# Kernel tuning notes

Hardware: AMD Instinct MI355X
Metric: run time of the kernel (lower is better)

## Reference

```python
import jax, jax.numpy as jnp
import numpy as np

SQRT2 = 1.4142135623730951
TARGET_DENSITY = 0.9
XL, YL, XH, YH = 0.0, 0.0, 1024.0, 1024.0
BSX, BSY = 2.0, 2.0
NM, NT, NF = 1_000_000, 10_000, 200_000
N_TOTAL = NM + NT + NF
NBX = int(round((XH - XL) / BSX))  # 512
NBY = int(round((YH - YL) / BSY))  # 512
K_MOV = 5   # ceil((max movable size 3 + 2*sqrt2*bs) / bs) with bs=2
K_FIX = 10  # ceil((max fixed size 16 + bs) / bs) with margin; extra bins overlap 0
PADDING = 1


def _splat(x, y, sx, sy, w, K):
    """Scatter-add exact rectangle/bin overlaps of each cell into a flat [NBX*NBY] map.
    x,y: lower-left corners [N]; sx,sy: sizes [N]; w: per-cell weight (ratio) [N]."""
    bx0 = jnp.floor((x - XL) / BSX).astype(jnp.int32)  # first impacted bin in x
    by0 = jnp.floor((y - YL) / BSY).astype(jnp.int32)
    ks = jnp.arange(K, dtype=jnp.int32)
    bx = bx0[:, None] + ks  # [N,K]
    by = by0[:, None] + ks
    ox = jnp.minimum(x[:, None] + sx[:, None], XL + (bx + 1) * BSX) - \
         jnp.maximum(x[:, None], XL + bx * BSX)
    oy = jnp.minimum(y[:, None] + sy[:, None], YL + (by + 1) * BSY) - \
         jnp.maximum(y[:, None], YL + by * BSY)
    ox = jnp.where((bx >= 0) & (bx < NBX), jnp.clip(ox, 0.0), 0.0)
    oy = jnp.where((by >= 0) & (by < NBY), jnp.clip(oy, 0.0), 0.0)
    bxc = jnp.clip(bx, 0, NBX - 1)
    byc = jnp.clip(by, 0, NBY - 1)
    v = w[:, None, None] * ox[:, :, None] * oy[:, None, :]        # [N,K,K]
    idx = (bxc[:, :, None] * NBY + byc[:, None, :]).reshape(-1)   # [N*K*K]
    return jnp.zeros(NBX * NBY, dtype=x.dtype).at[idx].add(v.reshape(-1))


def setup_inputs() -> dict:
    key = jax.random.key(0)
    k1, k2, k3, k4, k5, k6, k7, k8 = jax.random.split(key, 8)
    # node sizes: movable standard cells, fixed terminals (larger), fillers
    sx = jnp.concatenate([
        jax.random.uniform(k1, (NM,), minval=1.0, maxval=3.0),
        jax.random.uniform(k2, (NT,), minval=4.0, maxval=16.0),
        jax.random.uniform(k3, (NF,), minval=1.5, maxval=2.5)])
    sy = jnp.concatenate([
        jax.random.uniform(k4, (NM,), minval=1.0, maxval=3.0),
        jax.random.uniform(k5, (NT,), minval=4.0, maxval=16.0),
        jax.random.uniform(k6, (NF,), minval=1.5, maxval=2.5)])
    pos_x = jax.random.uniform(k7, (N_TOTAL,), minval=XL, maxval=XH - 16.0)
    pos_y = jax.random.uniform(k8, (N_TOTAL,), minval=YL, maxval=YH - 16.0)
    pos = jnp.concatenate([pos_x, pos_y])  # x coords then y coords
    return {"pos": pos, "node_size_x": sx, "node_size_y": sy}


def reference(pos, node_size_x, node_size_y):
    x = pos[:N_TOTAL]
    y = pos[N_TOTAL:]
    # --- initial density map from fixed terminals (exact overlap, no stretching) ---
    tsl = slice(NM, NM + NT)
    init_map = _splat(x[tsl], y[tsl], node_size_x[tsl], node_size_y[tsl],
                      jnp.ones((NT,), pos.dtype), K_FIX) * TARGET_DENSITY
    # --- movable + filler: stretch to >= bin_size*sqrt2, splat rescaled area ---
    sxc = jnp.maximum(node_size_x, BSX * SQRT2)
    syc = jnp.maximum(node_size_y, BSY * SQRT2)
    off_x = (node_size_x - sxc) * 0.5
    off_y = (node_size_y - syc) * 0.5
    ratio = (node_size_x * node_size_y) / (sxc * syc)
    mf = np.concatenate([np.arange(NM), np.arange(N_TOTAL - NF, N_TOTAL)])  # movable + filler
    dmap = init_map + _splat((x + off_x)[mf], (y + off_y)[mf], sxc[mf], syc[mf],
                             ratio[mf], K_MOV)
    dmap = dmap.reshape(NBX, NBY)
    # padding mask: border bins forced to target capacity
    bin_area = BSX * BSY
    ix = jnp.arange(NBX)
    iy = jnp.arange(NBY)
    pad = ((ix < PADDING) | (ix >= NBX - PADDING))[:, None] | \
          ((iy < PADDING) | (iy >= NBY - PADDING))[None, :]
    dmap = jnp.where(pad, TARGET_DENSITY * bin_area, dmap)
    density_cost = jnp.clip(dmap - TARGET_DENSITY * bin_area, 0.0).sum()[None]
    max_density = (dmap.max() / bin_area)[None]
    return density_cost, max_density
```

## Files before the change

kernel.cpp:

```cpp
#include <hip/hip_runtime.h>

#define NM_ 1000000
#define NT_ 10000
#define NF_ 200000
#define N_TOTAL_ 1210000
#define NBX_ 512
#define NBY_ 512
#define NBINS_ (NBX_ * NBY_)
#define TD_ 0.9f
#define PAD_VAL_ 3.6f
#define SQRT2x2_ 2.8284271247461903f

#define TSZ_ 16
#define TSH_ 4
#define TGX_ 32
#define NTILES_ 1024
#define HALO_ 2
#define TW_ 18
#define TAREA_ (TW_ * TW_)
#define CAPM_ 1536
#define CAPT_ 128
#define NB_ 512
#define NTH_ 512
#define CHUNK_ 2364
#define NGRP_ 8
#define QS_ 1024.0f
#define IQS_ (1.0f / 1024.0f)

static __device__ __forceinline__ int imin_(int a, int b) { return a < b ? a : b; }
static __device__ __forceinline__ int imax_(int a, int b) { return a > b ? a : b; }

static __device__ __forceinline__ void fadd_(float* p, float v) {
    unsafeAtomicAdd(p, v);
}

__global__ __launch_bounds__(NTH_) void count_kernel(
        const float* __restrict__ px, const float* __restrict__ py,
        const float* __restrict__ sxp, const float* __restrict__ syp,
        int* __restrict__ cnt, int* __restrict__ cntT) {
    __shared__ int hist[NTILES_];
    for (int t = threadIdx.x; t < NTILES_; t += blockDim.x) hist[t] = 0;
    if (blockIdx.x == 0)
        for (int t = threadIdx.x; t < NTILES_; t += blockDim.x) cntT[t] = 0;
    __syncthreads();
    int b = blockIdx.x;
    int lo = b * CHUNK_, hi = imin_(lo + CHUNK_, N_TOTAL_);
    for (int i = lo + threadIdx.x; i < hi; i += blockDim.x) {
        if (i >= NM_ && i < NM_ + NT_) continue;
        float sx0 = sxp[i], sy0 = syp[i];
        float sxc = fmaxf(sx0, SQRT2x2_);
        float syc = fmaxf(sy0, SQRT2x2_);
        float x = px[i] + (sx0 - sxc) * 0.5f;
        float y = py[i] + (sy0 - syc) * 0.5f;
        int bx0 = (int)floorf(x * 0.5f);
        int by0 = (int)floorf(y * 0.5f);
        int t = (imax_(bx0, 0) >> TSH_) * TGX_ + (imax_(by0, 0) >> TSH_);
        atomicAdd(&hist[t], 1);
    }
    __syncthreads();
    for (int t = threadIdx.x; t < NTILES_; t += blockDim.x)
        cnt[b * NTILES_ + t] = hist[t];
}

__global__ void scan_kernel(int* __restrict__ cnt, int* __restrict__ totM,
                            float* __restrict__ out) {
    int tile = blockIdx.x * 4 + (threadIdx.x >> 6);
    int l = threadIdx.x & 63;
    int X = l & 7;
    int mrow = l >> 3;
    int c[NGRP_];
#pragma unroll
    for (int g = 0; g < NGRP_; g++) c[g] = cnt[(l + 64 * g) * NTILES_ + tile];
    int off[NGRP_];
    int W = 0;
#pragma unroll
    for (int g = 0; g < NGRP_; g++) {
        int v = c[g];
#pragma unroll
        for (int s = 1; s < 8; s <<= 1) {
            int n = __shfl_up(v, 8 * s);
            if (mrow >= s) v += n;
        }
        off[g] = W + v - c[g];
        W += __shfl(v, X + 56);
    }
    int B = 0, tot = 0;
#pragma unroll
    for (int Xp = 0; Xp < 8; Xp++) {
        int t = __shfl(W, Xp);
        if (Xp < X) B += t;
        tot += t;
    }
#pragma unroll
    for (int g = 0; g < NGRP_; g++) cnt[(l + 64 * g) * NTILES_ + tile] = B + off[g];
    if (l == 0) totM[tile] = tot;
    if (blockIdx.x == 0 && threadIdx.x == 0) { out[0] = 0.0f; out[1] = 0.0f; }
}

__global__ __launch_bounds__(NTH_) void scatter_kernel(
        const float* __restrict__ px, const float* __restrict__ py,
        const float* __restrict__ sxp, const float* __restrict__ syp,
        const int* __restrict__ start, int* __restrict__ cntT,
        ushort4* __restrict__ recM, unsigned char* __restrict__ keyM,
        float4* __restrict__ recT) {
    __shared__ int cur[NTILES_];
    int b = blockIdx.x;
    for (int t = threadIdx.x; t < NTILES_; t += blockDim.x)
        cur[t] = start[b * NTILES_ + t];
    __syncthreads();
    int lo = b * CHUNK_, hi = imin_(lo + CHUNK_, N_TOTAL_);
    for (int i = lo + threadIdx.x; i < hi; i += blockDim.x) {
        float sx0 = sxp[i], sy0 = syp[i];
        bool fix = (i >= NM_) && (i < NM_ + NT_);
        if (!fix) {
            float sxc = fmaxf(sx0, SQRT2x2_);
            float syc = fmaxf(sy0, SQRT2x2_);
            float x = px[i] + (sx0 - sxc) * 0.5f;
            float y = py[i] + (sy0 - syc) * 0.5f;
            int bx0 = (int)floorf(x * 0.5f);
            int by0 = (int)floorf(y * 0.5f);
            int txo = (imax_(bx0, 0) >> TSH_) << TSH_;
            int tyo = (imax_(by0, 0) >> TSH_) << TSH_;
            int t = (txo >> TSH_) * TGX_ + (tyo >> TSH_);
            int slot = atomicAdd(&cur[t], 1);
            if (slot < CAPM_) {
                float bxo = txo * 2.0f - 16.0f;
                float byo = tyo * 2.0f - 16.0f;
                ushort4 q;
                q.x = (unsigned short)__float2int_rn((x - bxo) * QS_);
                q.y = (unsigned short)__float2int_rn((y - byo) * QS_);
                q.z = (unsigned short)__float2int_rn(sx0 * QS_);
                q.w = (unsigned short)__float2int_rn(sy0 * QS_);
                recM[(size_t)t * CAPM_ + slot] = q;
                int kr = imin_(imax_(bx0 - txo, 0), 15);
                int kc = imin_(imax_(by0 - tyo, 0), 15);
                keyM[(size_t)t * CAPM_ + slot] = (unsigned char)(kr * 16 + kc);
            }
        } else {
            float x = px[i], y = py[i];
            int bx0 = (int)floorf(x * 0.5f);
            int by0 = (int)floorf(y * 0.5f);
            int bxm = imin_((int)floorf((x + sx0) * 0.5f), NBX_ - 1);
            int bym = imin_((int)floorf((y + sy0) * 0.5f), NBY_ - 1);
            int txA = bx0 >> TSH_, txB = bxm >> TSH_;
            int tyA = by0 >> TSH_, tyB = bym >> TSH_;
            for (int tx = txA; tx <= txB; tx++)
                for (int ty = tyA; ty <= tyB; ty++) {
                    int t = tx * TGX_ + ty;
                    int slot = atomicAdd(&cntT[t], 1);
                    if (slot < CAPT_) recT[(size_t)t * CAPT_ + slot] = make_float4(x, y, sx0, sy0);
                }
        }
    }
}

__global__ __launch_bounds__(512) void accumS_kernel(
        const ushort4* __restrict__ recM, const unsigned char* __restrict__ keyM,
        const float4* __restrict__ recT,
        const int* __restrict__ totM, const int* __restrict__ cntT,
        float* __restrict__ tiles) {
    __shared__ float4 srec[CAPM_];
    __shared__ float  sw[CAPM_];
    __shared__ float  m[TAREA_];
    __shared__ int    boff[257];
    __shared__ int    bcur[256];
    int tile = blockIdx.x;
    int tx16 = (tile >> 5) << TSH_;
    int ty16 = (tile & (TGX_ - 1)) << TSH_;
    for (int k = threadIdx.x; k < TAREA_; k += 512) m[k] = 0.0f;
    if (threadIdx.x < 256) bcur[threadIdx.x] = 0;
    __syncthreads();
    int nM = imin_(totM[tile], CAPM_);
    const ushort4* rq = recM + (size_t)tile * CAPM_;
    const unsigned char* kM = keyM + (size_t)tile * CAPM_;
    for (int i = threadIdx.x; i < nM; i += 512)
        atomicAdd(&bcur[kM[i]], 1);
    __syncthreads();
    if (threadIdx.x < 64) {
        int l = threadIdx.x;
        int c0 = bcur[4 * l], c1 = bcur[4 * l + 1], c2 = bcur[4 * l + 2], c3 = bcur[4 * l + 3];
        int s = c0 + c1 + c2 + c3;
        int incl = s;
#pragma unroll
        for (int off = 1; off < 64; off <<= 1) {
            int n = __shfl_up(incl, off);
            if (l >= off) incl += n;
        }
        int run = incl - s;
        boff[4 * l] = run;
        boff[4 * l + 1] = run + c0;
        boff[4 * l + 2] = run + c0 + c1;
        boff[4 * l + 3] = run + c0 + c1 + c2;
        if (l == 63) boff[256] = incl;
    }
    __syncthreads();
    if (threadIdx.x < 256) bcur[threadIdx.x] = boff[threadIdx.x];
    __syncthreads();
    float bxo = tx16 * 2.0f - 16.0f;
    float byo = ty16 * 2.0f - 16.0f;
    for (int i = threadIdx.x; i < nM; i += 512) {
        ushort4 q = rq[i];
        float x = bxo + q.x * IQS_;
        float y = byo + q.y * IQS_;
        float sx0 = q.z * IQS_, sy0 = q.w * IQS_;
        float sxc = fmaxf(sx0, SQRT2x2_);
        float syc = fmaxf(sy0, SQRT2x2_);
        float w = (sx0 * sy0) / (sxc * syc);
        int slot = atomicAdd(&bcur[kM[i]], 1);
        srec[slot] = make_float4(x, y, x + sxc, y + syc);
        sw[slot] = w;
    }
    int nT = imin_(cntT[tile], CAPT_);
    const float4* rT = recT + (size_t)tile * CAPT_;
    for (int i = threadIdx.x; i < nT; i += 512) {
        float4 r = rT[i];
        float xe = r.x + r.z, ye = r.y + r.w;
        int bx0 = (int)floorf(r.x * 0.5f);
        int by0 = (int)floorf(r.y * 0.5f);
        int bxA = imax_(bx0, tx16), byA = imax_(by0, ty16);
        int bxB = imin_(imin_((int)floorf(xe * 0.5f), tx16 + TSZ_ - 1), NBX_ - 1);
        int byB = imin_(imin_((int)floorf(ye * 0.5f), ty16 + TSZ_ - 1), NBY_ - 1);
        for (int bx = bxA; bx <= bxB; bx++) {
            float ox = fminf(xe, (bx + 1) * 2.0f) - fmaxf(r.x, bx * 2.0f);
            ox = fmaxf(ox, 0.0f) * TD_;
            for (int by = byA; by <= byB; by++) {
                float oy = fminf(ye, (by + 1) * 2.0f) - fmaxf(r.y, by * 2.0f);
                atomicAdd(&m[(bx - tx16) * TW_ + (by - ty16)], ox * fmaxf(oy, 0.0f));
            }
        }
    }
    __syncthreads();
    if (threadIdx.x < TAREA_) {
        int r = threadIdx.x / TW_;
        int c = threadIdx.x % TW_;
        float blx = (tx16 + r) * 2.0f, bhx = blx + 2.0f;
        float bly = (ty16 + c) * 2.0f, bhy = bly + 2.0f;
        int krA = imax_(r - 2, 0), krB = imin_(r, 15);
        int kcA = imax_(c - 2, 0), kcB = imin_(c, 15);
        float acc = 0.0f;
        for (int kr = krA; kr <= krB; kr++) {
            int j0 = boff[kr * 16 + kcA];
            int j1 = boff[kr * 16 + kcB + 1];
            for (int j = j0; j < j1; j++) {
                float4 t = srec[j];
                float ox = fminf(t.z, bhx) - fmaxf(t.x, blx);
                float oy = fminf(t.w, bhy) - fmaxf(t.y, bly);
                acc = fmaf(sw[j], fmaxf(ox, 0.0f) * fmaxf(oy, 0.0f), acc);
            }
        }
        m[threadIdx.x] += acc;
    }
    __syncthreads();
    for (int k = threadIdx.x; k < TAREA_; k += 512)
        tiles[(size_t)tile * TAREA_ + k] = m[k];
}

__global__ void reduce2_kernel(const float* __restrict__ tiles, float* __restrict__ out) {
    float sum = 0.0f, mx = 0.0f;
    for (int i = blockIdx.x * blockDim.x + threadIdx.x; i < NBINS_;
         i += gridDim.x * blockDim.x) {
        int gx = i >> 9, gy = i & (NBY_ - 1);
        float v;
        bool pad = (gx < 1) | (gx >= NBX_ - 1) | (gy < 1) | (gy >= NBY_ - 1);
        if (pad) {
            v = PAD_VAL_;
        } else {
            int tx = gx >> TSH_, lx = gx & (TSZ_ - 1);
            int ty = gy >> TSH_, ly = gy & (TSZ_ - 1);
            v = tiles[(size_t)(tx * TGX_ + ty) * TAREA_ + lx * TW_ + ly];
            if (lx < HALO_ && tx > 0)
                v += tiles[(size_t)((tx - 1) * TGX_ + ty) * TAREA_ + (lx + TSZ_) * TW_ + ly];
            if (ly < HALO_ && ty > 0)
                v += tiles[(size_t)(tx * TGX_ + (ty - 1)) * TAREA_ + lx * TW_ + (ly + TSZ_)];
            if (lx < HALO_ && ly < HALO_ && tx > 0 && ty > 0)
                v += tiles[(size_t)((tx - 1) * TGX_ + (ty - 1)) * TAREA_ + (lx + TSZ_) * TW_ + (ly + TSZ_)];
        }
        sum += fmaxf(v - PAD_VAL_, 0.0f);
        mx = fmaxf(mx, v);
    }
#pragma unroll
    for (int off = 32; off > 0; off >>= 1) {
        sum += __shfl_down(sum, off);
        mx = fmaxf(mx, __shfl_down(mx, off));
    }
    __shared__ float ssum[8], smx[8];
    int lane = threadIdx.x & 63, wid = threadIdx.x >> 6;
    if (lane == 0) { ssum[wid] = sum; smx[wid] = mx; }
    __syncthreads();
    if (threadIdx.x == 0) {
        int nw = blockDim.x >> 6;
        float s = 0.0f, m = 0.0f;
        for (int w = 0; w < nw; w++) { s += ssum[w]; m = fmaxf(m, smx[w]); }
        fadd_(&out[0], s);
        atomicMax((unsigned int*)&out[1], __float_as_uint(m * 0.25f));
    }
}

__global__ void zero_kernel(float* __restrict__ dmap, float* __restrict__ out) {
    int i = blockIdx.x * blockDim.x + threadIdx.x;
    if (i < NBINS_) dmap[i] = 0.0f;
    if (i == 0) { out[0] = 0.0f; out[1] = 0.0f; }
}

__global__ void splat_fix(const float* __restrict__ px, const float* __restrict__ py,
                          const float* __restrict__ sxp, const float* __restrict__ syp,
                          float* __restrict__ dmap) {
    int t = blockIdx.x * blockDim.x + threadIdx.x;
    if (t >= NT_) return;
    int i = NM_ + t;
    float x = px[i], y = py[i], sx = sxp[i], sy = syp[i];
    int bx0 = (int)floorf(x * 0.5f), by0 = (int)floorf(y * 0.5f);
    for (int kx = 0; kx < 10; kx++) {
        int bx = bx0 + kx;
        if (bx < 0 || bx >= NBX_) continue;
        float ox = fminf(x + sx, (bx + 1) * 2.0f) - fmaxf(x, bx * 2.0f);
        if (ox <= 0.0f) continue;
        for (int ky = 0; ky < 10; ky++) {
            int by = by0 + ky;
            if (by < 0 || by >= NBY_) continue;
            float oy = fminf(y + sy, (by + 1) * 2.0f) - fmaxf(y, by * 2.0f);
            if (oy <= 0.0f) continue;
            fadd_(&dmap[bx * NBY_ + by], TD_ * ox * oy);
        }
    }
}

__global__ void splat_mov(const float* __restrict__ px, const float* __restrict__ py,
                          const float* __restrict__ sxp, const float* __restrict__ syp,
                          float* __restrict__ dmap) {
    int i = blockIdx.x * blockDim.x + threadIdx.x;
    if (i >= N_TOTAL_) return;
    if (i >= NM_ && i < NM_ + NT_) return;
    float sx = sxp[i], sy = syp[i];
    float sxc = fmaxf(sx, SQRT2x2_), syc = fmaxf(sy, SQRT2x2_);
    float x = px[i] + (sx - sxc) * 0.5f, y = py[i] + (sy - syc) * 0.5f;
    float w = (sx * sy) / (sxc * syc);
    int bx0 = (int)floorf(x * 0.5f), by0 = (int)floorf(y * 0.5f);
    for (int kx = 0; kx < 5; kx++) {
        int bx = bx0 + kx;
        if (bx < 0 || bx >= NBX_) continue;
        float ox = fminf(x + sxc, (bx + 1) * 2.0f) - fmaxf(x, bx * 2.0f);
        if (ox <= 0.0f) continue;
        for (int ky = 0; ky < 5; ky++) {
            int by = by0 + ky;
            if (by < 0 || by >= NBY_) continue;
            float oy = fminf(y + syc, (by + 1) * 2.0f) - fmaxf(y, by * 2.0f);
            if (oy <= 0.0f) continue;
            fadd_(&dmap[bx * NBY_ + by], w * ox * oy);
        }
    }
}

__global__ void reduce_kernel(const float* __restrict__ dmap, float* __restrict__ out) {
    float sum = 0.0f, mx = 0.0f;
    for (int i = blockIdx.x * blockDim.x + threadIdx.x; i < NBINS_;
         i += gridDim.x * blockDim.x) {
        int ix = i >> 9, iy = i & (NBY_ - 1);
        float v = dmap[i];
        bool pad = (ix < 1) | (ix >= NBX_ - 1) | (iy < 1) | (iy >= NBY_ - 1);
        if (pad) v = PAD_VAL_;
        sum += fmaxf(v - PAD_VAL_, 0.0f);
        mx = fmaxf(mx, v);
    }
#pragma unroll
    for (int off = 32; off > 0; off >>= 1) {
        sum += __shfl_down(sum, off);
        mx = fmaxf(mx, __shfl_down(mx, off));
    }
    __shared__ float ssum[8], smx[8];
    int lane = threadIdx.x & 63, wid = threadIdx.x >> 6;
    if (lane == 0) { ssum[wid] = sum; smx[wid] = mx; }
    __syncthreads();
    if (threadIdx.x == 0) {
        int nw = blockDim.x >> 6;
        float s = 0.0f, m = 0.0f;
        for (int w = 0; w < nw; w++) { s += ssum[w]; m = fmaxf(m, smx[w]); }
        fadd_(&out[0], s);
        atomicMax((unsigned int*)&out[1], __float_as_uint(m * 0.25f));
    }
}

extern "C" void kernel_launch(void* const* d_in, const int* in_sizes, int n_in,
                              void* d_out, int out_size, void* d_ws, size_t ws_size,
                              hipStream_t stream) {
    const float* pos = (const float*)d_in[0];
    const float* nsx = (const float*)d_in[1];
    const float* nsy = (const float*)d_in[2];
    const float* px = pos;
    const float* py = pos + N_TOTAL_;
    float* out = (float*)d_out;

    size_t o_cnt   = 0;
    size_t o_totM  = o_cnt + (size_t)NB_ * NTILES_ * 4;
    size_t o_cntT  = o_totM + (size_t)NTILES_ * 4;
    size_t o_recM  = o_cntT + (size_t)NTILES_ * 4;
    size_t o_keyM  = o_recM + (size_t)NTILES_ * CAPM_ * 8;
    size_t o_recT  = o_keyM + (size_t)NTILES_ * CAPM_;
    size_t o_tiles = o_recT + (size_t)NTILES_ * CAPT_ * 16;
    size_t req     = o_tiles + (size_t)NTILES_ * TAREA_ * 4;

    if (ws_size >= req) {
        char* ws = (char*)d_ws;
        int*           cnt   = (int*)(ws + o_cnt);
        int*           totM  = (int*)(ws + o_totM);
        int*           cntT  = (int*)(ws + o_cntT);
        ushort4*       recM  = (ushort4*)(ws + o_recM);
        unsigned char* keyM  = (unsigned char*)(ws + o_keyM);
        float4*        recT  = (float4*)(ws + o_recT);
        float*         tiles = (float*)(ws + o_tiles);

        count_kernel<<<NB_, NTH_, 0, stream>>>(px, py, nsx, nsy, cnt, cntT);
        scan_kernel<<<NTILES_ / 4, 256, 0, stream>>>(cnt, totM, out);
        scatter_kernel<<<NB_, NTH_, 0, stream>>>(px, py, nsx, nsy, cnt, cntT, recM, keyM, recT);
        accumS_kernel<<<NTILES_, 512, 0, stream>>>(recM, keyM, recT, totM, cntT, tiles);
        reduce2_kernel<<<1024, 256, 0, stream>>>(tiles, out);
    } else {
        float* dmap = (float*)d_ws;
        zero_kernel<<<(NBINS_ + 255) / 256, 256, 0, stream>>>(dmap, out);
        splat_fix<<<(NT_ + 255) / 256, 256, 0, stream>>>(px, py, nsx, nsy, dmap);
        splat_mov<<<(N_TOTAL_ + 255) / 256, 256, 0, stream>>>(px, py, nsx, nsy, dmap);
        reduce_kernel<<<1024, 256, 0, stream>>>(dmap, out);
    }
}
```

Before: 91.40 us.

## Replace count+scan+scatter with single-pass per-block segmented tile buckets

```diff
diff --git a/kernel.cpp b/kernel.cpp
--- a/kernel.cpp
+++ b/kernel.cpp
@@ -23,7 +23,7 @@
 #define NB_ 512
 #define NTH_ 512
 #define CHUNK_ 2364
-#define NGRP_ 8
+#define SEGC_ 16
 #define QS_ 1024.0f
 #define IQS_ (1.0f / 1024.0f)
 
@@ -34,80 +34,21 @@
     unsafeAtomicAdd(p, v);
 }
 
-__global__ __launch_bounds__(NTH_) void count_kernel(
+__global__ void zero0_kernel(int* __restrict__ cntT, float* __restrict__ out) {
+    int i = blockIdx.x * blockDim.x + threadIdx.x;
+    if (i < NTILES_) cntT[i] = 0;
+    if (i == 0) { out[0] = 0.0f; out[1] = 0.0f; }
+}
+
+__global__ __launch_bounds__(NTH_) void scatter1_kernel(
         const float* __restrict__ px, const float* __restrict__ py,
         const float* __restrict__ sxp, const float* __restrict__ syp,
-        int* __restrict__ cnt, int* __restrict__ cntT) {
-    __shared__ int hist[NTILES_];
-    for (int t = threadIdx.x; t < NTILES_; t += blockDim.x) hist[t] = 0;
-    if (blockIdx.x == 0)
-        for (int t = threadIdx.x; t < NTILES_; t += blockDim.x) cntT[t] = 0;
+        int* __restrict__ cnt, int* __restrict__ cntT,
+        ushort4* __restrict__ recM, float4* __restrict__ recT) {
+    __shared__ int cur[NTILES_];
+    for (int t = threadIdx.x; t < NTILES_; t += blockDim.x) cur[t] = 0;
     __syncthreads();
     int b = blockIdx.x;
-    int lo = b * CHUNK_, hi = imin_(lo + CHUNK_, N_TOTAL_);
-    for (int i = lo + threadIdx.x; i < hi; i += blockDim.x) {
-        if (i >= NM_ && i < NM_ + NT_) continue;
-        float sx0 = sxp[i], sy0 = syp[i];
-        float sxc = fmaxf(sx0, SQRT2x2_);
-        float syc = fmaxf(sy0, SQRT2x2_);
-        float x = px[i] + (sx0 - sxc) * 0.5f;
-        float y = py[i] + (sy0 - syc) * 0.5f;
-        int bx0 = (int)floorf(x * 0.5f);
-        int by0 = (int)floorf(y * 0.5f);
-        int t = (imax_(bx0, 0) >> TSH_) * TGX_ + (imax_(by0, 0) >> TSH_);
-        atomicAdd(&hist[t], 1);
-    }
-    __syncthreads();
-    for (int t = threadIdx.x; t < NTILES_; t += blockDim.x)
-        cnt[b * NTILES_ + t] = hist[t];
-}
-
-__global__ void scan_kernel(int* __restrict__ cnt, int* __restrict__ totM,
-                            float* __restrict__ out) {
-    int tile = blockIdx.x * 4 + (threadIdx.x >> 6);
-    int l = threadIdx.x & 63;
-    int X = l & 7;
-    int mrow = l >> 3;
-    int c[NGRP_];
-#pragma unroll
-    for (int g = 0; g < NGRP_; g++) c[g] = cnt[(l + 64 * g) * NTILES_ + tile];
-    int off[NGRP_];
-    int W = 0;
-#pragma unroll
-    for (int g = 0; g < NGRP_; g++) {
-        int v = c[g];
-#pragma unroll
-        for (int s = 1; s < 8; s <<= 1) {
-            int n = __shfl_up(v, 8 * s);
-            if (mrow >= s) v += n;
-        }
-        off[g] = W + v - c[g];
-        W += __shfl(v, X + 56);
-    }
-    int B = 0, tot = 0;
-#pragma unroll
-    for (int Xp = 0; Xp < 8; Xp++) {
-        int t = __shfl(W, Xp);
-        if (Xp < X) B += t;
-        tot += t;
-    }
-#pragma unroll
-    for (int g = 0; g < NGRP_; g++) cnt[(l + 64 * g) * NTILES_ + tile] = B + off[g];
-    if (l == 0) totM[tile] = tot;
-    if (blockIdx.x == 0 && threadIdx.x == 0) { out[0] = 0.0f; out[1] = 0.0f; }
-}
-
-__global__ __launch_bounds__(NTH_) void scatter_kernel(
-        const float* __restrict__ px, const float* __restrict__ py,
-        const float* __restrict__ sxp, const float* __restrict__ syp,
-        const int* __restrict__ start, int* __restrict__ cntT,
-        ushort4* __restrict__ recM, unsigned char* __restrict__ keyM,
-        float4* __restrict__ recT) {
-    __shared__ int cur[NTILES_];
-    int b = blockIdx.x;
-    for (int t = threadIdx.x; t < NTILES_; t += blockDim.x)
-        cur[t] = start[b * NTILES_ + t];
-    __syncthreads();
     int lo = b * CHUNK_, hi = imin_(lo + CHUNK_, N_TOTAL_);
     for (int i = lo + threadIdx.x; i < hi; i += blockDim.x) {
         float sx0 = sxp[i], sy0 = syp[i];
@@ -123,7 +64,7 @@
             int tyo = (imax_(by0, 0) >> TSH_) << TSH_;
             int t = (txo >> TSH_) * TGX_ + (tyo >> TSH_);
             int slot = atomicAdd(&cur[t], 1);
-            if (slot < CAPM_) {
+            if (slot < SEGC_) {
                 float bxo = txo * 2.0f - 16.0f;
                 float byo = tyo * 2.0f - 16.0f;
                 ushort4 q;
@@ -131,10 +72,7 @@
                 q.y = (unsigned short)__float2int_rn((y - byo) * QS_);
                 q.z = (unsigned short)__float2int_rn(sx0 * QS_);
                 q.w = (unsigned short)__float2int_rn(sy0 * QS_);
-                recM[(size_t)t * CAPM_ + slot] = q;
-                int kr = imin_(imax_(bx0 - txo, 0), 15);
-                int kc = imin_(imax_(by0 - tyo, 0), 15);
-                keyM[(size_t)t * CAPM_ + slot] = (unsigned char)(kr * 16 + kc);
+                recM[((size_t)t * NB_ + b) * SEGC_ + slot] = q;
             }
         } else {
             float x = px[i], y = py[i];
@@ -152,29 +90,40 @@
                 }
         }
     }
-}
-
-__global__ __launch_bounds__(512) void accumS_kernel(
-        const ushort4* __restrict__ recM, const unsigned char* __restrict__ keyM,
-        const float4* __restrict__ recT,
-        const int* __restrict__ totM, const int* __restrict__ cntT,
+    __syncthreads();
+    for (int t = threadIdx.x; t < NTILES_; t += blockDim.x)
+        cnt[b * NTILES_ + t] = imin_(cur[t], SEGC_);
+}
+
+__global__ __launch_bounds__(512) void accumSeg_kernel(
+        const ushort4* __restrict__ recM, const float4* __restrict__ recT,
+        const int* __restrict__ cnt, const int* __restrict__ cntT,
         float* __restrict__ tiles) {
     __shared__ float4 srec[CAPM_];
     __shared__ float  sw[CAPM_];
     __shared__ float  m[TAREA_];
     __shared__ int    boff[257];
     __shared__ int    bcur[256];
+    __shared__ unsigned char scnt[NB_];
     int tile = blockIdx.x;
     int tx16 = (tile >> 5) << TSH_;
     int ty16 = (tile & (TGX_ - 1)) << TSH_;
     for (int k = threadIdx.x; k < TAREA_; k += 512) m[k] = 0.0f;
     if (threadIdx.x < 256) bcur[threadIdx.x] = 0;
-    __syncthreads();
-    int nM = imin_(totM[tile], CAPM_);
-    const ushort4* rq = recM + (size_t)tile * CAPM_;
-    const unsigned char* kM = keyM + (size_t)tile * CAPM_;
-    for (int i = threadIdx.x; i < nM; i += 512)
-        atomicAdd(&bcur[kM[i]], 1);
+    if (threadIdx.x < NB_) scnt[threadIdx.x] = (unsigned char)cnt[threadIdx.x * NTILES_ + tile];
+    __syncthreads();
+    const ushort4* seg0 = recM + (size_t)tile * NB_ * SEGC_;
+    {
+        int b = threadIdx.x;
+        int c = scnt[b];
+        const ushort4* p = seg0 + b * SEGC_;
+        for (int j = 0; j < c; j++) {
+            ushort4 q = p[j];
+            int kr = imin_(imax_((q.x >> 11) - 8, 0), 15);
+            int kc = imin_(imax_((q.y >> 11) - 8, 0), 15);
+            atomicAdd(&bcur[kr * 16 + kc], 1);
+        }
+    }
     __syncthreads();
     if (threadIdx.x < 64) {
         int l = threadIdx.x;
@@ -198,17 +147,26 @@
     __syncthreads();
     float bxo = tx16 * 2.0f - 16.0f;
     float byo = ty16 * 2.0f - 16.0f;
-    for (int i = threadIdx.x; i < nM; i += 512) {
-        ushort4 q = rq[i];
-        float x = bxo + q.x * IQS_;
-        float y = byo + q.y * IQS_;
-        float sx0 = q.z * IQS_, sy0 = q.w * IQS_;
-        float sxc = fmaxf(sx0, SQRT2x2_);
-        float syc = fmaxf(sy0, SQRT2x2_);
-        float w = (sx0 * sy0) / (sxc * syc);
-        int slot = atomicAdd(&bcur[kM[i]], 1);
-        srec[slot] = make_float4(x, y, x + sxc, y + syc);
-        sw[slot] = w;
+    {
+        int b = threadIdx.x;
+        int c = scnt[b];
+        const ushort4* p = seg0 + b * SEGC_;
+        for (int j = 0; j < c; j++) {
+            ushort4 q = p[j];
+            int kr = imin_(imax_((q.x >> 11) - 8, 0), 15);
+            int kc = imin_(imax_((q.y >> 11) - 8, 0), 15);
+            float x = bxo + q.x * IQS_;
+            float y = byo + q.y * IQS_;
+            float sx0 = q.z * IQS_, sy0 = q.w * IQS_;
+            float sxc = fmaxf(sx0, SQRT2x2_);
+            float syc = fmaxf(sy0, SQRT2x2_);
+            float w = (sx0 * sy0) / (sxc * syc);
+            int slot = atomicAdd(&bcur[kr * 16 + kc], 1);
+            if (slot < CAPM_) {
+                srec[slot] = make_float4(x, y, x + sxc, y + syc);
+                sw[slot] = w;
+            }
+        }
     }
     int nT = imin_(cntT[tile], CAPT_);
     const float4* rT = recT + (size_t)tile * CAPT_;
@@ -239,8 +197,8 @@
         int kcA = imax_(c - 2, 0), kcB = imin_(c, 15);
         float acc = 0.0f;
         for (int kr = krA; kr <= krB; kr++) {
-            int j0 = boff[kr * 16 + kcA];
-            int j1 = boff[kr * 16 + kcB + 1];
+            int j0 = imin_(boff[kr * 16 + kcA], CAPM_);
+            int j1 = imin_(boff[kr * 16 + kcB + 1], CAPM_);
             for (int j = j0; j < j1; j++) {
                 float4 t = srec[j];
                 float ox = fminf(t.z, bhx) - fmaxf(t.x, blx);
@@ -391,28 +349,23 @@
     float* out = (float*)d_out;
 
     size_t o_cnt   = 0;
-    size_t o_totM  = o_cnt + (size_t)NB_ * NTILES_ * 4;
-    size_t o_cntT  = o_totM + (size_t)NTILES_ * 4;
+    size_t o_cntT  = o_cnt + (size_t)NB_ * NTILES_ * 4;
     size_t o_recM  = o_cntT + (size_t)NTILES_ * 4;
-    size_t o_keyM  = o_recM + (size_t)NTILES_ * CAPM_ * 8;
-    size_t o_recT  = o_keyM + (size_t)NTILES_ * CAPM_;
+    size_t o_recT  = o_recM + (size_t)NTILES_ * NB_ * SEGC_ * 8;
     size_t o_tiles = o_recT + (size_t)NTILES_ * CAPT_ * 16;
     size_t req     = o_tiles + (size_t)NTILES_ * TAREA_ * 4;
 
     if (ws_size >= req) {
         char* ws = (char*)d_ws;
-        int*           cnt   = (int*)(ws + o_cnt);
-        int*           totM  = (int*)(ws + o_totM);
-        int*           cntT  = (int*)(ws + o_cntT);
-        ushort4*       recM  = (ushort4*)(ws + o_recM);
-        unsigned char* keyM  = (unsigned char*)(ws + o_keyM);
-        float4*        recT  = (float4*)(ws + o_recT);
-        float*         tiles = (float*)(ws + o_tiles);
-
-        count_kernel<<<NB_, NTH_, 0, stream>>>(px, py, nsx, nsy, cnt, cntT);
-        scan_kernel<<<NTILES_ / 4, 256, 0, stream>>>(cnt, totM, out);
-        scatter_kernel<<<NB_, NTH_, 0, stream>>>(px, py, nsx, nsy, cnt, cntT, recM, keyM, recT);
-        accumS_kernel<<<NTILES_, 512, 0, stream>>>(recM, keyM, recT, totM, cntT, tiles);
+        int*     cnt   = (int*)(ws + o_cnt);
+        int*     cntT  = (int*)(ws + o_cntT);
+        ushort4* recM  = (ushort4*)(ws + o_recM);
+        float4*  recT  = (float4*)(ws + o_recT);
+        float*   tiles = (float*)(ws + o_tiles);
+
+        zero0_kernel<<<4, 256, 0, stream>>>(cntT, out);
+        scatter1_kernel<<<NB_, NTH_, 0, stream>>>(px, py, nsx, nsy, cnt, cntT, recM, recT);
+        accumSeg_kernel<<<NTILES_, 512, 0, stream>>>(recM, recT, cnt, cntT, tiles);
         reduce2_kernel<<<1024, 256, 0, stream>>>(tiles, out);
     } else {
         float* dmap = (float*)d_ws;
```

Result: slower. 102.6 us (+12.3%).

## Split scatter into movable and fixed kernels, derive bin keys from quantized records

Applied to the files above, without the earlier changes.

```diff
diff --git a/kernel.cpp b/kernel.cpp
--- a/kernel.cpp
+++ b/kernel.cpp
@@ -34,14 +34,18 @@
     unsafeAtomicAdd(p, v);
 }
 
+__global__ void zero0_kernel(int* __restrict__ cntT, float* __restrict__ out) {
+    int i = blockIdx.x * blockDim.x + threadIdx.x;
+    if (i < NTILES_) cntT[i] = 0;
+    if (i == 0) { out[0] = 0.0f; out[1] = 0.0f; }
+}
+
 __global__ __launch_bounds__(NTH_) void count_kernel(
         const float* __restrict__ px, const float* __restrict__ py,
         const float* __restrict__ sxp, const float* __restrict__ syp,
-        int* __restrict__ cnt, int* __restrict__ cntT) {
+        int* __restrict__ cnt) {
     __shared__ int hist[NTILES_];
     for (int t = threadIdx.x; t < NTILES_; t += blockDim.x) hist[t] = 0;
-    if (blockIdx.x == 0)
-        for (int t = threadIdx.x; t < NTILES_; t += blockDim.x) cntT[t] = 0;
     __syncthreads();
     int b = blockIdx.x;
     int lo = b * CHUNK_, hi = imin_(lo + CHUNK_, N_TOTAL_);
@@ -62,8 +66,7 @@
         cnt[b * NTILES_ + t] = hist[t];
 }
 
-__global__ void scan_kernel(int* __restrict__ cnt, int* __restrict__ totM,
-                            float* __restrict__ out) {
+__global__ void scan_kernel(int* __restrict__ cnt, int* __restrict__ totM) {
     int tile = blockIdx.x * 4 + (threadIdx.x >> 6);
     int l = threadIdx.x & 63;
     int X = l & 7;
@@ -94,71 +97,73 @@
 #pragma unroll
     for (int g = 0; g < NGRP_; g++) cnt[(l + 64 * g) * NTILES_ + tile] = B + off[g];
     if (l == 0) totM[tile] = tot;
-    if (blockIdx.x == 0 && threadIdx.x == 0) { out[0] = 0.0f; out[1] = 0.0f; }
-}
-
-__global__ __launch_bounds__(NTH_) void scatter_kernel(
+}
+
+__global__ __launch_bounds__(NTH_) void scatterM_kernel(
         const float* __restrict__ px, const float* __restrict__ py,
         const float* __restrict__ sxp, const float* __restrict__ syp,
-        const int* __restrict__ start, int* __restrict__ cntT,
-        ushort4* __restrict__ recM, unsigned char* __restrict__ keyM,
-        float4* __restrict__ recT) {
+        const int* __restrict__ start, ushort4* __restrict__ recM) {
     __shared__ int cur[NTILES_];
     int b = blockIdx.x;
     for (int t = threadIdx.x; t < NTILES_; t += blockDim.x)
         cur[t] = start[b * NTILES_ + t];
     __syncthreads();
     int lo = b * CHUNK_, hi = imin_(lo + CHUNK_, N_TOTAL_);
-    for (int i = lo + threadIdx.x; i < hi; i += blockDim.x) {
+#pragma unroll 2
+    for (int i = lo + threadIdx.x; i < hi; i += NTH_) {
+        if (i >= NM_ && i < NM_ + NT_) continue;
         float sx0 = sxp[i], sy0 = syp[i];
-        bool fix = (i >= NM_) && (i < NM_ + NT_);
-        if (!fix) {
-            float sxc = fmaxf(sx0, SQRT2x2_);
-            float syc = fmaxf(sy0, SQRT2x2_);
-            float x = px[i] + (sx0 - sxc) * 0.5f;
-            float y = py[i] + (sy0 - syc) * 0.5f;
-            int bx0 = (int)floorf(x * 0.5f);
-            int by0 = (int)floorf(y * 0.5f);
-            int txo = (imax_(bx0, 0) >> TSH_) << TSH_;
-            int tyo = (imax_(by0, 0) >> TSH_) << TSH_;
-            int t = (txo >> TSH_) * TGX_ + (tyo >> TSH_);
-            int slot = atomicAdd(&cur[t], 1);
-            if (slot < CAPM_) {
-                float bxo = txo * 2.0f - 16.0f;
-                float byo = tyo * 2.0f - 16.0f;
-                ushort4 q;
-                q.x = (unsigned short)__float2int_rn((x - bxo) * QS_);
-                q.y = (unsigned short)__float2int_rn((y - byo) * QS_);
-                q.z = (unsigned short)__float2int_rn(sx0 * QS_);
-                q.w = (unsigned short)__float2int_rn(sy0 * QS_);
-                recM[(size_t)t * CAPM_ + slot] = q;
-                int kr = imin_(imax_(bx0 - txo, 0), 15);
-                int kc = imin_(imax_(by0 - tyo, 0), 15);
-                keyM[(size_t)t * CAPM_ + slot] = (unsigned char)(kr * 16 + kc);
-            }
-        } else {
-            float x = px[i], y = py[i];
-            int bx0 = (int)floorf(x * 0.5f);
-            int by0 = (int)floorf(y * 0.5f);
-            int bxm = imin_((int)floorf((x + sx0) * 0.5f), NBX_ - 1);
-            int bym = imin_((int)floorf((y + sy0) * 0.5f), NBY_ - 1);
-            int txA = bx0 >> TSH_, txB = bxm >> TSH_;
-            int tyA = by0 >> TSH_, tyB = bym >> TSH_;
-            for (int tx = txA; tx <= txB; tx++)
-                for (int ty = tyA; ty <= tyB; ty++) {
-                    int t = tx * TGX_ + ty;
-                    int slot = atomicAdd(&cntT[t], 1);
-                    if (slot < CAPT_) recT[(size_t)t * CAPT_ + slot] = make_float4(x, y, sx0, sy0);
-                }
-        }
-    }
+        float sxc = fmaxf(sx0, SQRT2x2_);
+        float syc = fmaxf(sy0, SQRT2x2_);
+        float x = px[i] + (sx0 - sxc) * 0.5f;
+        float y = py[i] + (sy0 - syc) * 0.5f;
+        int bx0 = (int)floorf(x * 0.5f);
+        int by0 = (int)floorf(y * 0.5f);
+        int txo = (imax_(bx0, 0) >> TSH_) << TSH_;
+        int tyo = (imax_(by0, 0) >> TSH_) << TSH_;
+        int t = (txo >> TSH_) * TGX_ + (tyo >> TSH_);
+        int slot = atomicAdd(&cur[t], 1);
+        if (slot < CAPM_) {
+            float bxo = txo * 2.0f - 16.0f;
+            float byo = tyo * 2.0f - 16.0f;
+            ushort4 q;
+            q.x = (unsigned short)__float2int_rn((x - bxo) * QS_);
+            q.y = (unsigned short)__float2int_rn((y - byo) * QS_);
+            q.z = (unsigned short)__float2int_rn(sx0 * QS_);
+            q.w = (unsigned short)__float2int_rn(sy0 * QS_);
+            recM[(size_t)t * CAPM_ + slot] = q;
+        }
+    }
+}
+
+__global__ void scatterT_kernel(
+        const float* __restrict__ px, const float* __restrict__ py,
+        const float* __restrict__ sxp, const float* __restrict__ syp,
+        int* __restrict__ cntT, float4* __restrict__ recT) {
+    int k = blockIdx.x * blockDim.x + threadIdx.x;
+    if (k >= NT_) return;
+    int i = NM_ + k;
+    float x = px[i], y = py[i];
+    float sx0 = sxp[i], sy0 = syp[i];
+    int bx0 = (int)floorf(x * 0.5f);
+    int by0 = (int)floorf(y * 0.5f);
+    int bxm = imin_((int)floorf((x + sx0) * 0.5f), NBX_ - 1);
+    int bym = imin_((int)floorf((y + sy0) * 0.5f), NBY_ - 1);
+    int txA = bx0 >> TSH_, txB = bxm >> TSH_;
+    int tyA = by0 >> TSH_, tyB = bym >> TSH_;
+    for (int tx = txA; tx <= txB; tx++)
+        for (int ty = tyA; ty <= tyB; ty++) {
+            int t = tx * TGX_ + ty;
+            int slot = atomicAdd(&cntT[t], 1);
+            if (slot < CAPT_) recT[(size_t)t * CAPT_ + slot] = make_float4(x, y, sx0, sy0);
+        }
 }
 
 __global__ __launch_bounds__(512) void accumS_kernel(
-        const ushort4* __restrict__ recM, const unsigned char* __restrict__ keyM,
-        const float4* __restrict__ recT,
+        const ushort4* __restrict__ recM, const float4* __restrict__ recT,
         const int* __restrict__ totM, const int* __restrict__ cntT,
         float* __restrict__ tiles) {
+    __shared__ ushort4 raw[CAPM_];
     __shared__ float4 srec[CAPM_];
     __shared__ float  sw[CAPM_];
     __shared__ float  m[TAREA_];
@@ -172,9 +177,13 @@
     __syncthreads();
     int nM = imin_(totM[tile], CAPM_);
     const ushort4* rq = recM + (size_t)tile * CAPM_;
-    const unsigned char* kM = keyM + (size_t)tile * CAPM_;
-    for (int i = threadIdx.x; i < nM; i += 512)
-        atomicAdd(&bcur[kM[i]], 1);
+    for (int i = threadIdx.x; i < nM; i += 512) {
+        ushort4 q = rq[i];
+        raw[i] = q;
+        int kr = imin_(imax_((q.x >> 11) - 8, 0), 15);
+        int kc = imin_(imax_((q.y >> 11) - 8, 0), 15);
+        atomicAdd(&bcur[kr * 16 + kc], 1);
+    }
     __syncthreads();
     if (threadIdx.x < 64) {
         int l = threadIdx.x;
@@ -199,14 +208,16 @@
     float bxo = tx16 * 2.0f - 16.0f;
     float byo = ty16 * 2.0f - 16.0f;
     for (int i = threadIdx.x; i < nM; i += 512) {
-        ushort4 q = rq[i];
+        ushort4 q = raw[i];
+        int kr = imin_(imax_((q.x >> 11) - 8, 0), 15);
+        int kc = imin_(imax_((q.y >> 11) - 8, 0), 15);
         float x = bxo + q.x * IQS_;
         float y = byo + q.y * IQS_;
         float sx0 = q.z * IQS_, sy0 = q.w * IQS_;
         float sxc = fmaxf(sx0, SQRT2x2_);
         float syc = fmaxf(sy0, SQRT2x2_);
         float w = (sx0 * sy0) / (sxc * syc);
-        int slot = atomicAdd(&bcur[kM[i]], 1);
+        int slot = atomicAdd(&bcur[kr * 16 + kc], 1);
         srec[slot] = make_float4(x, y, x + sxc, y + syc);
         sw[slot] = w;
     }
@@ -394,25 +405,25 @@
     size_t o_totM  = o_cnt + (size_t)NB_ * NTILES_ * 4;
     size_t o_cntT  = o_totM + (size_t)NTILES_ * 4;
     size_t o_recM  = o_cntT + (size_t)NTILES_ * 4;
-    size_t o_keyM  = o_recM + (size_t)NTILES_ * CAPM_ * 8;
-    size_t o_recT  = o_keyM + (size_t)NTILES_ * CAPM_;
+    size_t o_recT  = o_recM + (size_t)NTILES_ * CAPM_ * 8;
     size_t o_tiles = o_recT + (size_t)NTILES_ * CAPT_ * 16;
     size_t req     = o_tiles + (size_t)NTILES_ * TAREA_ * 4;
 
     if (ws_size >= req) {
         char* ws = (char*)d_ws;
-        int*           cnt   = (int*)(ws + o_cnt);
-        int*           totM  = (int*)(ws + o_totM);
-        int*           cntT  = (int*)(ws + o_cntT);
-        ushort4*       recM  = (ushort4*)(ws + o_recM);
-        unsigned char* keyM  = (unsigned char*)(ws + o_keyM);
-        float4*        recT  = (float4*)(ws + o_recT);
-        float*         tiles = (float*)(ws + o_tiles);
-
-        count_kernel<<<NB_, NTH_, 0, stream>>>(px, py, nsx, nsy, cnt, cntT);
-        scan_kernel<<<NTILES_ / 4, 256, 0, stream>>>(cnt, totM, out);
-        scatter_kernel<<<NB_, NTH_, 0, stream>>>(px, py, nsx, nsy, cnt, cntT, recM, keyM, recT);
-        accumS_kernel<<<NTILES_, 512, 0, stream>>>(recM, keyM, recT, totM, cntT, tiles);
+        int*     cnt   = (int*)(ws + o_cnt);
+        int*     totM  = (int*)(ws + o_totM);
+        int*     cntT  = (int*)(ws + o_cntT);
+        ushort4* recM  = (ushort4*)(ws + o_recM);
+        float4*  recT  = (float4*)(ws + o_recT);
+        float*   tiles = (float*)(ws + o_tiles);
+
+        zero0_kernel<<<4, 256, 0, stream>>>(cntT, out);
+        count_kernel<<<NB_, NTH_, 0, stream>>>(px, py, nsx, nsy, cnt);
+        scan_kernel<<<NTILES_ / 4, 256, 0, stream>>>(cnt, totM);
+        scatterM_kernel<<<NB_, NTH_, 0, stream>>>(px, py, nsx, nsy, cnt, recM);
+        scatterT_kernel<<<(NT_ + 255) / 256, 256, 0, stream>>>(px, py, nsx, nsy, cntT, recT);
+        accumS_kernel<<<NTILES_, 512, 0, stream>>>(recM, recT, totM, cntT, tiles);
         reduce2_kernel<<<1024, 256, 0, stream>>>(tiles, out);
     } else {
         float* dmap = (float*)d_ws;
```

Result: slower. 96.71 us (+5.8%).
